# Optimization experiments

Hardware: AMD Instinct MI355X
Metric: run time of the kernel (lower is better)

Reference implementation:

```python
import jax, jax.numpy as jnp
import numpy as np

EPS = 1e-8
NUM_HEADS = 8


def setup_inputs() -> dict:
    key = jax.random.key(0)
    ks = jax.random.split(key, 12)
    B, T, F = 8, 512, 512
    H = NUM_HEADS
    dh = F // H
    maxlen = 2048
    s = 0.02  # weight init scale
    inp = {
        "x": jax.random.normal(ks[0], (B, T, F), jnp.float32),
        "Wq": jax.random.normal(ks[1], (F, F), jnp.float32) * s,
        "bq": jax.random.normal(ks[2], (F,), jnp.float32) * s,
        "Wk": jax.random.normal(ks[3], (F, F), jnp.float32) * s,
        "bk": jax.random.normal(ks[4], (F,), jnp.float32) * s,
        "Wv": jax.random.normal(ks[5], (F, F), jnp.float32) * s,
        "bv": jax.random.normal(ks[6], (F,), jnp.float32) * s,
        "Wo": jax.random.normal(ks[7], (F, F), jnp.float32) * s,
        "bo": jax.random.normal(ks[8], (F,), jnp.float32) * s,
        "delta": jnp.ones((1,), jnp.float32),
        "cache_k": jax.random.normal(ks[9], (B * H, maxlen, dh), jnp.float32) * 0.1,
        "cache_v": jax.random.normal(ks[10], (B * H, maxlen, dh), jnp.float32) * 0.1,
    }
    return inp


def _split_heads(t, H):
    # torch.cat(torch.split(t, dh, dim=-1), dim=0): head index outermost on dim 0
    B, T, F = t.shape
    dh = F // H
    return t.reshape(B, T, H, dh).transpose(2, 0, 1, 3).reshape(H * B, T, dh)


def _merge_heads(t, H):
    HB, T, dh = t.shape
    B = HB // H
    return t.reshape(H, B, T, dh).transpose(1, 2, 0, 3).reshape(B, T, H * dh)


def reference(x, Wq, bq, Wk, bk, Wv, bv, Wo, bo, delta, cache_k, cache_v):
    B, T, F = x.shape
    H = NUM_HEADS
    maxlen = cache_k.shape[1]
    d = jnp.sqrt(jnp.asarray(F, jnp.float32))

    q = _split_heads(x @ Wq.T + bq, H)  # [H*B, T, dh]
    k = _split_heads(x @ Wk.T + bk, H)
    v = _split_heads(x @ Wv.T + bv, H)

    # rolling KV cache: drop oldest T, append new T -> length maxlen
    k_full = jnp.concatenate([cache_k[:, T:], k], axis=1)  # [H*B, maxlen, dh]
    v_full = jnp.concatenate([cache_v[:, T:], v], axis=1)

    # Gaussian positional bias G = exp(-(i-j)^2 / (delta^2 + EPS)), last T rows
    i = jnp.arange(maxlen, dtype=jnp.float32)
    ind = -(i[:, None] - i[None, :]) ** 2  # [maxlen, maxlen]
    G = jnp.exp(ind[-T:] / (delta[0] ** 2 + EPS))  # [T, maxlen]

    scores = jnp.abs(jnp.einsum('btd,bsd->bts', q, k_full) * G / d)
    attn = jax.nn.softmax(scores, axis=-1)  # [H*B, T, maxlen]
    o = jnp.einsum('bts,bsd->btd', attn, v_full)  # [H*B, T, dh]

    out = _merge_heads(o, H) @ Wo.T + bo  # [B, T, F]
    return out
```

## Files before the change

kernel.cpp:

```cpp
#include <hip/hip_runtime.h>
#include <cstdint>
#include <cstddef>


typedef _Float16 f16x8 __attribute__((ext_vector_type(8)));
typedef _Float16 f16x4 __attribute__((ext_vector_type(4)));
typedef float f32x4 __attribute__((ext_vector_type(4)));

#define GLOBAL_AS __attribute__((address_space(1)))
#define LDS_AS __attribute__((address_space(3)))

__global__ void convert_f32_f16(const float* __restrict__ x,
                                const float* __restrict__ w0,
                                const float* __restrict__ w1,
                                const float* __restrict__ w2,
                                const float* __restrict__ w3,
                                _Float16* __restrict__ dst) {
  long e = ((long)blockIdx.x * 256 + threadIdx.x) * 4;
  const float* src;
  long off;
  if (e < 2097152) { src = x; off = 0; }
  else {
    int seg = (int)((e - 2097152) >> 18);
    src = seg == 0 ? w0 : seg == 1 ? w1 : seg == 2 ? w2 : w3;
    off = 2097152 + ((long)seg << 18);
  }
  float4 v = *(const float4*)(src + (e - off));
  f16x4 h;
  h[0] = (_Float16)v.x; h[1] = (_Float16)v.y;
  h[2] = (_Float16)v.z; h[3] = (_Float16)v.w;
  *(f16x4*)(dst + e) = h;
}

template <int MODE>
__launch_bounds__(256)
__global__ void gemm_nt(const _Float16* __restrict__ A,
                        const _Float16* __restrict__ B0,
                        const _Float16* __restrict__ B1,
                        const _Float16* __restrict__ B2,
                        const float* __restrict__ bias0,
                        const float* __restrict__ bias1,
                        const float* __restrict__ bias2,
                        void* out0v, void* out1v, void* out2v,
                        int K) {
  __shared__ __align__(16) _Float16 As[128 * 32];
  __shared__ __align__(16) _Float16 Bs[128 * 32];
  const int tid = threadIdx.x;
  const int m0 = blockIdx.x * 128;
  const int n0g = blockIdx.y * 128;

  const _Float16* Bsel;
  const float* bsel;
  void* oselv;
  int nloc0;
  if (MODE == 0) {
    int which = n0g >> 9;
    Bsel = which == 0 ? B0 : which == 1 ? B1 : B2;
    bsel = which == 0 ? bias0 : which == 1 ? bias1 : bias2;
    oselv = which == 0 ? out0v : which == 1 ? out1v : out2v;
    nloc0 = n0g & 511;
  } else {
    Bsel = B0; bsel = bias0; oselv = out0v; nloc0 = n0g;
  }

  const int w = tid >> 6, lane = tid & 63;
  const int wm = (w & 1) * 64, wn = (w >> 1) * 64;

  f32x4 acc[4][4];
#pragma unroll
  for (int i = 0; i < 4; i++)
#pragma unroll
    for (int j = 0; j < 4; j++) acc[i][j] = (f32x4){0.f, 0.f, 0.f, 0.f};

  for (int k0 = 0; k0 < K; k0 += 32) {
    __syncthreads();
#pragma unroll
    for (int r = 0; r < 2; r++) {
      int chunk = r * 256 + tid;
      int row = chunk >> 2;
      int c = (chunk & 3) * 8;
      const _Float16* ga = A + (size_t)(m0 + row) * K + k0 + c;
      const _Float16* gb = Bsel + (size_t)(nloc0 + row) * K + k0 + c;
      __builtin_amdgcn_global_load_lds((const GLOBAL_AS void*)ga,
                                       (LDS_AS void*)(As + chunk * 8), 16, 0, 0);
      __builtin_amdgcn_global_load_lds((const GLOBAL_AS void*)gb,
                                       (LDS_AS void*)(Bs + chunk * 8), 16, 0, 0);
    }
    __syncthreads();

    f16x8 af[4], bf[4];
#pragma unroll
    for (int i = 0; i < 4; i++) {
      af[i] = *(const f16x8*)(As + (wm + i * 16 + (lane & 15)) * 32 + (lane >> 4) * 8);
      bf[i] = *(const f16x8*)(Bs + (wn + i * 16 + (lane & 15)) * 32 + (lane >> 4) * 8);
    }
#pragma unroll
    for (int i = 0; i < 4; i++)
#pragma unroll
      for (int j = 0; j < 4; j++)
        acc[i][j] = __builtin_amdgcn_mfma_f32_16x16x32_f16(af[i], bf[j], acc[i][j], 0, 0, 0);
  }

  const int mbase = m0 + wm + ((lane >> 4) << 2);
  const int nbase = nloc0 + wn + (lane & 15);
#pragma unroll
  for (int i = 0; i < 4; i++) {
#pragma unroll
    for (int j = 0; j < 4; j++) {
      int fg = nbase + j * 16;
      float bv = bsel[fg];
#pragma unroll
      for (int r = 0; r < 4; r++) {
        int m = mbase + i * 16 + r;
        float val = acc[i][j][r] + bv;
        if (MODE == 0) {
          int h = fg >> 6, dd = fg & 63, b = m >> 9, t = m & 511;
          ((_Float16*)oselv)[(((size_t)((h << 3) + b) * 512 + t) << 6) + dd] =
              (_Float16)val;
        } else {
          ((float*)oselv)[(size_t)m * 512 + fg] = val;
        }
      }
    }
  }
}

__global__ void sum_v_partial(const float* __restrict__ cache_v,
                              const _Float16* __restrict__ v_new,
                              float* __restrict__ S_v) {
  const int hb = blockIdx.x;
  const int r0 = blockIdx.y * 128;
  const int d = threadIdx.x & 63, p = threadIdx.x >> 6;
  float s = 0.f;
#pragma unroll 8
  for (int r = r0 + p; r < r0 + 128; r += 4) {
    if (r < 1536)
      s += cache_v[((size_t)hb * 2048 + r + 512) * 64 + d];
    else
      s += (float)v_new[((size_t)hb * 512 + (r - 1536)) * 64 + d];
  }
  __shared__ float red[256];
  red[threadIdx.x] = s;
  __syncthreads();
  if (p == 0)
    atomicAdd(&S_v[hb * 64 + d], red[d] + red[64 + d] + red[128 + d] + red[192 + d]);
}

__launch_bounds__(256)
__global__ void attn_mfma(const _Float16* __restrict__ q,
                          const _Float16* __restrict__ k_new,
                          const _Float16* __restrict__ v_new,
                          const float* __restrict__ cache_k,
                          const float* __restrict__ cache_v,
                          const float* __restrict__ S_v,
                          const float* __restrict__ delta,
                          _Float16* __restrict__ o_merged) {
  const int hb = blockIdx.y;
  const int t0 = blockIdx.x * 64;
  const int jlo_t = 1520 + t0;

  __shared__ __align__(16) _Float16 Q_sh[64 * 72];
  __shared__ __align__(16) _Float16 K_sh[96 * 72];
  __shared__ __align__(16) _Float16 VT_sh[64 * 104];
  __shared__ __align__(16) _Float16 P_sh[64 * 104];
  __shared__ float S_sh[64 * 101];
  __shared__ float G_sh[40];
  __shared__ float pm_sh[256], ps_sh[256], em_sh[64], id_sh[64];

  const int tid = threadIdx.x;
  const int w = tid >> 6, lane = tid & 63;
  const float dscale = 0.044194173824159216f;

  if (tid < 36) {
    int di = tid - 16;
    float inv_g = 1.0f / (delta[0] * delta[0] + 1e-8f);
    G_sh[tid] = (tid <= 32) ? expf(-(float)(di * di) * inv_g) : 0.f;
  }
#pragma unroll
  for (int it = 0; it < 2; it++) {
    int idx = it * 256 + tid;
    int r = idx >> 3, c8 = (idx & 7) * 8;
    *(f16x8*)(Q_sh + r * 72 + c8) =
        *(const f16x8*)(q + ((size_t)hb * 512 + t0 + r) * 64 + c8);
  }
#pragma unroll
  for (int it = 0; it < 3; it++) {
    int idx = it * 256 + tid;
    int r = idx >> 3, c8 = (idx & 7) * 8;
    int j = jlo_t + r;
    f16x8 kh, vh;
    if (j < 1536) {
      const float* kp = cache_k + ((size_t)hb * 2048 + j + 512) * 64 + c8;
      const float* vp = cache_v + ((size_t)hb * 2048 + j + 512) * 64 + c8;
#pragma unroll
      for (int e = 0; e < 8; e++) {
        kh[e] = (_Float16)kp[e];
        vh[e] = (_Float16)vp[e];
      }
    } else if (j < 2048) {
      kh = *(const f16x8*)(k_new + ((size_t)hb * 512 + (j - 1536)) * 64 + c8);
      vh = *(const f16x8*)(v_new + ((size_t)hb * 512 + (j - 1536)) * 64 + c8);
    } else {
#pragma unroll
      for (int e = 0; e < 8; e++) { kh[e] = (_Float16)0.f; vh[e] = (_Float16)0.f; }
    }
    *(f16x8*)(K_sh + r * 72 + c8) = kh;
#pragma unroll
    for (int e = 0; e < 8; e++) VT_sh[(c8 + e) * 104 + r] = vh[e];
  }
  for (int idx = tid; idx < 832; idx += 256) {
    int r = idx / 13, c = (idx % 13) * 8;
    *(f16x8*)(P_sh + r * 104 + c) = (f16x8){0, 0, 0, 0, 0, 0, 0, 0};
  }
  __syncthreads();

  {
    const int mrow = w * 16 + (lane & 15);
    const int koff = (lane >> 4) * 8;
    f16x8 aq0 = *(const f16x8*)(Q_sh + mrow * 72 + koff);
    f16x8 aq1 = *(const f16x8*)(Q_sh + mrow * 72 + 32 + koff);
    f32x4 accS[6];
#pragma unroll
    for (int n = 0; n < 6; n++) accS[n] = (f32x4){0.f, 0.f, 0.f, 0.f};
#pragma unroll
    for (int n = 0; n < 6; n++) {
      f16x8 b0 = *(const f16x8*)(K_sh + (n * 16 + (lane & 15)) * 72 + koff);
      f16x8 b1 = *(const f16x8*)(K_sh + (n * 16 + (lane & 15)) * 72 + 32 + koff);
      accS[n] = __builtin_amdgcn_mfma_f32_16x16x32_f16(aq0, b0, accS[n], 0, 0, 0);
      accS[n] = __builtin_amdgcn_mfma_f32_16x16x32_f16(aq1, b1, accS[n], 0, 0, 0);
    }
#pragma unroll
    for (int n = 0; n < 6; n++)
#pragma unroll
      for (int r = 0; r < 4; r++) {
        int tl = w * 16 + ((lane >> 4) << 2) + r;
        int jb = n * 16 + (lane & 15);
        S_sh[tl * 101 + jb] = fabsf(accS[n][r]) * dscale;
      }
  }
  __syncthreads();

  {
    const int tl = lane;
    const int jmax = 2047 - (jlo_t + tl);
    float s[9];
    float pm = 0.f;
#pragma unroll
    for (int jj = 0; jj < 9; jj++) {
      int off = w * 9 + jj;
      bool valid = (off <= 32) && (off <= jmax);
      s[jj] = valid ? S_sh[tl * 101 + tl + off] * G_sh[off] : 0.f;
      pm = fmaxf(pm, s[jj]);
    }
    pm_sh[w * 64 + tl] = pm;
    __syncthreads();
    float m = fmaxf(fmaxf(pm_sh[tl], pm_sh[64 + tl]),
                    fmaxf(pm_sh[128 + tl], pm_sh[192 + tl]));
    float em = expf(-m);
    float ps = 0.f;
#pragma unroll
    for (int jj = 0; jj < 9; jj++) {
      int off = w * 9 + jj;
      bool valid = (off <= 32) && (off <= jmax);
      float wgt = valid ? (expf(s[jj] - m) - em) : 0.f;
      ps += wgt;
      if (valid) P_sh[tl * 104 + tl + off] = (_Float16)wgt;
    }
    ps_sh[w * 64 + tl] = ps;
    __syncthreads();
    if (w == 0) {
      float sw = ps_sh[tl] + ps_sh[64 + tl] + ps_sh[128 + tl] + ps_sh[192 + tl];
      em_sh[tl] = em;
      id_sh[tl] = 1.0f / (sw + 2048.f * em);
    }
  }

  f32x4 accO[4];
#pragma unroll
  for (int mi = 0; mi < 4; mi++) accO[mi] = (f32x4){0.f, 0.f, 0.f, 0.f};
  {
    const int koff = (lane >> 4) * 8;
    const int nrow = w * 16 + (lane & 15);
#pragma unroll
    for (int k = 0; k < 3; k++) {
      f16x8 bv = *(const f16x8*)(VT_sh + nrow * 104 + k * 32 + koff);
#pragma unroll
      for (int mi = 0; mi < 4; mi++) {
        f16x8 ap = *(const f16x8*)(P_sh + (mi * 16 + (lane & 15)) * 104 + k * 32 + koff);
        accO[mi] = __builtin_amdgcn_mfma_f32_16x16x32_f16(ap, bv, accO[mi], 0, 0, 0);
      }
    }
  }
  __syncthreads();

  const int h = hb >> 3, b = hb & 7;
  const int d = w * 16 + (lane & 15);
  const float svd = S_v[hb * 64 + d];
#pragma unroll
  for (int mi = 0; mi < 4; mi++)
#pragma unroll
    for (int r = 0; r < 4; r++) {
      int trow = mi * 16 + ((lane >> 4) << 2) + r;
      float val = (accO[mi][r] + em_sh[trow] * svd) * id_sh[trow];
      o_merged[((size_t)(b * 512 + t0 + trow)) * 512 + h * 64 + d] = (_Float16)val;
    }
}

extern "C" void kernel_launch(void* const* d_in, const int* in_sizes, int n_in,
                              void* d_out, int out_size, void* d_ws, size_t ws_size,
                              hipStream_t stream) {
  const float* x = (const float*)d_in[0];
  const float* Wq = (const float*)d_in[1];
  const float* bq = (const float*)d_in[2];
  const float* Wk = (const float*)d_in[3];
  const float* bk = (const float*)d_in[4];
  const float* Wv = (const float*)d_in[5];
  const float* bv = (const float*)d_in[6];
  const float* Wo = (const float*)d_in[7];
  const float* bo = (const float*)d_in[8];
  const float* delta = (const float*)d_in[9];
  const float* cache_k = (const float*)d_in[10];
  const float* cache_v = (const float*)d_in[11];
  float* out = (float*)d_out;

  _Float16* xh = (_Float16*)d_ws;
  _Float16* Wqh = xh + 2097152;
  _Float16* Wkh = Wqh + 262144;
  _Float16* Wvh = Wkh + 262144;
  _Float16* Woh = Wvh + 262144;
  _Float16* qf = Woh + 262144;
  _Float16* kf = qf + 2097152;
  _Float16* vf = kf + 2097152;
  float* sv = (float*)(vf + 2097152);
  _Float16* oh = (_Float16*)(sv + 4096);

  convert_f32_f16<<<3072, 256, 0, stream>>>(x, Wq, Wk, Wv, Wo, xh);

  dim3 g1(32, 12);
  gemm_nt<0><<<g1, 256, 0, stream>>>(xh, Wqh, Wkh, Wvh, bq, bk, bv,
                                     (void*)qf, (void*)kf, (void*)vf, 512);

  hipMemsetAsync(sv, 0, 64 * 64 * sizeof(float), stream);
  dim3 gs(64, 16);
  sum_v_partial<<<gs, 256, 0, stream>>>(cache_v, vf, sv);

  dim3 g2(8, 64);
  attn_mfma<<<g2, 256, 0, stream>>>(qf, kf, vf, cache_k, cache_v, sv, delta, oh);

  dim3 g3(32, 4);
  gemm_nt<1><<<g3, 256, 0, stream>>>(oh, Woh, nullptr, nullptr, bo, nullptr, nullptr,
                                     (void*)out, nullptr, nullptr, 512);
}
```

Before: 170.0 us.

## Fuse cache_v sum into prep kernel, shrink GEMM tiles, drop atomics and memset

The conversion kernel now also computes partial sums of the cached V rows, written to per-chunk slots rather than accumulated with atomics. This removes the memset, and a small kernel sums the new V rows after the QKV GEMM. The attention kernel reduces the 20 partials itself and loads the K/V tail with float4 reads. Both GEMMs use smaller N tiles (and a 64x64 tile for the output projection), giving more blocks to fill the GPU. The risk is lower per-block data reuse in the GEMMs and extra partial-reduction work in every attention block.

```diff
diff --git a/kernel.cpp b/kernel.cpp
--- a/kernel.cpp
+++ b/kernel.cpp
@@ -10,140 +10,141 @@
 #define GLOBAL_AS __attribute__((address_space(1)))
 #define LDS_AS __attribute__((address_space(3)))
 
-__global__ void convert_f32_f16(const float* __restrict__ x,
-                                const float* __restrict__ w0,
-                                const float* __restrict__ w1,
-                                const float* __restrict__ w2,
-                                const float* __restrict__ w3,
-                                _Float16* __restrict__ dst) {
-  long e = ((long)blockIdx.x * 256 + threadIdx.x) * 4;
-  const float* src;
-  long off;
-  if (e < 2097152) { src = x; off = 0; }
-  else {
-    int seg = (int)((e - 2097152) >> 18);
-    src = seg == 0 ? w0 : seg == 1 ? w1 : seg == 2 ? w2 : w3;
-    off = 2097152 + ((long)seg << 18);
-  }
-  float4 v = *(const float4*)(src + (e - off));
-  f16x4 h;
-  h[0] = (_Float16)v.x; h[1] = (_Float16)v.y;
-  h[2] = (_Float16)v.z; h[3] = (_Float16)v.w;
-  *(f16x4*)(dst + e) = h;
-}
-
-template <int MODE>
 __launch_bounds__(256)
-__global__ void gemm_nt(const _Float16* __restrict__ A,
-                        const _Float16* __restrict__ B0,
-                        const _Float16* __restrict__ B1,
-                        const _Float16* __restrict__ B2,
-                        const float* __restrict__ bias0,
-                        const float* __restrict__ bias1,
-                        const float* __restrict__ bias2,
-                        void* out0v, void* out1v, void* out2v,
-                        int K) {
-  __shared__ __align__(16) _Float16 As[128 * 32];
-  __shared__ __align__(16) _Float16 Bs[128 * 32];
+__global__ void prep(const float* __restrict__ x,
+                     const float* __restrict__ Wq, const float* __restrict__ Wk,
+                     const float* __restrict__ Wv, const float* __restrict__ Wo,
+                     const float* __restrict__ cache_v,
+                     _Float16* __restrict__ xh, _Float16* __restrict__ wh,
+                     float* __restrict__ part) {
+  const int bid = blockIdx.x;
   const int tid = threadIdx.x;
-  const int m0 = blockIdx.x * 128;
-  const int n0g = blockIdx.y * 128;
-
-  const _Float16* Bsel;
-  const float* bsel;
-  void* oselv;
-  int nloc0;
-  if (MODE == 0) {
-    int which = n0g >> 9;
-    Bsel = which == 0 ? B0 : which == 1 ? B1 : B2;
-    bsel = which == 0 ? bias0 : which == 1 ? bias1 : bias2;
-    oselv = which == 0 ? out0v : which == 1 ? out1v : out2v;
-    nloc0 = n0g & 511;
+  if (bid < 2048) {
+    long e = ((long)bid * 256 + tid) * 4;
+    float4 v = *(const float4*)(x + e);
+    f16x4 h;
+    h[0] = (_Float16)v.x; h[1] = (_Float16)v.y;
+    h[2] = (_Float16)v.z; h[3] = (_Float16)v.w;
+    *(f16x4*)(xh + e) = h;
+  } else if (bid < 3072) {
+    long e = ((long)(bid - 2048) * 256 + tid) * 4;
+    int seg = (int)(e >> 18);
+    const float* w = seg == 0 ? Wq : seg == 1 ? Wk : seg == 2 ? Wv : Wo;
+    float4 v = *(const float4*)(w + (e & 262143));
+    f16x4 h;
+    h[0] = (_Float16)v.x; h[1] = (_Float16)v.y;
+    h[2] = (_Float16)v.z; h[3] = (_Float16)v.w;
+    *(f16x4*)(wh + e) = h;
   } else {
-    Bsel = B0; bsel = bias0; oselv = out0v; nloc0 = n0g;
-  }
-
-  const int w = tid >> 6, lane = tid & 63;
-  const int wm = (w & 1) * 64, wn = (w >> 1) * 64;
-
-  f32x4 acc[4][4];
-#pragma unroll
-  for (int i = 0; i < 4; i++)
-#pragma unroll
-    for (int j = 0; j < 4; j++) acc[i][j] = (f32x4){0.f, 0.f, 0.f, 0.f};
-
-  for (int k0 = 0; k0 < K; k0 += 32) {
-    __syncthreads();
-#pragma unroll
-    for (int r = 0; r < 2; r++) {
-      int chunk = r * 256 + tid;
-      int row = chunk >> 2;
-      int c = (chunk & 3) * 8;
-      const _Float16* ga = A + (size_t)(m0 + row) * K + k0 + c;
-      const _Float16* gb = Bsel + (size_t)(nloc0 + row) * K + k0 + c;
-      __builtin_amdgcn_global_load_lds((const GLOBAL_AS void*)ga,
-                                       (LDS_AS void*)(As + chunk * 8), 16, 0, 0);
-      __builtin_amdgcn_global_load_lds((const GLOBAL_AS void*)gb,
-                                       (LDS_AS void*)(Bs + chunk * 8), 16, 0, 0);
-    }
-    __syncthreads();
-
-    f16x8 af[4], bf[4];
-#pragma unroll
-    for (int i = 0; i < 4; i++) {
-      af[i] = *(const f16x8*)(As + (wm + i * 16 + (lane & 15)) * 32 + (lane >> 4) * 8);
-      bf[i] = *(const f16x8*)(Bs + (wn + i * 16 + (lane & 15)) * 32 + (lane >> 4) * 8);
-    }
-#pragma unroll
-    for (int i = 0; i < 4; i++)
-#pragma unroll
-      for (int j = 0; j < 4; j++)
-        acc[i][j] = __builtin_amdgcn_mfma_f32_16x16x32_f16(af[i], bf[j], acc[i][j], 0, 0, 0);
-  }
-
-  const int mbase = m0 + wm + ((lane >> 4) << 2);
-  const int nbase = nloc0 + wn + (lane & 15);
-#pragma unroll
-  for (int i = 0; i < 4; i++) {
-#pragma unroll
-    for (int j = 0; j < 4; j++) {
-      int fg = nbase + j * 16;
-      float bv = bsel[fg];
-#pragma unroll
-      for (int r = 0; r < 4; r++) {
-        int m = mbase + i * 16 + r;
-        float val = acc[i][j][r] + bv;
-        if (MODE == 0) {
-          int h = fg >> 6, dd = fg & 63, b = m >> 9, t = m & 511;
-          ((_Float16*)oselv)[(((size_t)((h << 3) + b) * 512 + t) << 6) + dd] =
-              (_Float16)val;
-        } else {
-          ((float*)oselv)[(size_t)m * 512 + fg] = val;
-        }
-      }
-    }
-  }
-}
-
-__global__ void sum_v_partial(const float* __restrict__ cache_v,
-                              const _Float16* __restrict__ v_new,
-                              float* __restrict__ S_v) {
-  const int hb = blockIdx.x;
-  const int r0 = blockIdx.y * 128;
-  const int d = threadIdx.x & 63, p = threadIdx.x >> 6;
+    int pb = bid - 3072;
+    int hb = pb >> 4, chunk = pb & 15;
+    int d = tid & 63, p = tid >> 6;
+    int r0 = 512 + chunk * 96;
+    float s = 0.f;
+    for (int r = r0 + p; r < r0 + 96; r += 4)
+      s += cache_v[((size_t)hb * 2048 + r) * 64 + d];
+    __shared__ float red[256];
+    red[tid] = s;
+    __syncthreads();
+    if (p == 0)
+      part[(hb * 20 + chunk) * 64 + d] =
+          red[d] + red[64 + d] + red[128 + d] + red[192 + d];
+  }
+}
+
+__launch_bounds__(256)
+__global__ void sumv_new(const _Float16* __restrict__ v_new,
+                         float* __restrict__ part) {
+  int hb = blockIdx.x >> 2, chunk = blockIdx.x & 3;
+  int d = threadIdx.x & 63, p = threadIdx.x >> 6;
+  int r0 = chunk * 128;
   float s = 0.f;
-#pragma unroll 8
-  for (int r = r0 + p; r < r0 + 128; r += 4) {
-    if (r < 1536)
-      s += cache_v[((size_t)hb * 2048 + r + 512) * 64 + d];
-    else
-      s += (float)v_new[((size_t)hb * 512 + (r - 1536)) * 64 + d];
-  }
+  for (int r = r0 + p; r < r0 + 128; r += 4)
+    s += (float)v_new[((size_t)hb * 512 + r) * 64 + d];
   __shared__ float red[256];
   red[threadIdx.x] = s;
   __syncthreads();
   if (p == 0)
-    atomicAdd(&S_v[hb * 64 + d], red[d] + red[64 + d] + red[128 + d] + red[192 + d]);
+    part[(hb * 20 + 16 + chunk) * 64 + d] =
+        red[d] + red[64 + d] + red[128 + d] + red[192 + d];
+}
+
+__launch_bounds__(256)
+__global__ void gemm_qkv(const _Float16* __restrict__ xh,
+                         const _Float16* __restrict__ wh,
+                         const float* __restrict__ bq,
+                         const float* __restrict__ bk,
+                         const float* __restrict__ bv,
+                         _Float16* __restrict__ q, _Float16* __restrict__ k,
+                         _Float16* __restrict__ v) {
+  __shared__ __align__(16) _Float16 As[128 * 32];
+  __shared__ __align__(16) _Float16 Bs[64 * 32];
+  const int tid = threadIdx.x;
+  const int m0 = blockIdx.x * 128;
+  const int n0g = blockIdx.y * 64;
+  const int which = n0g >> 9;
+  const int nloc0 = n0g & 511;
+  const _Float16* Bsel = wh + (size_t)which * 262144;
+  const float* bsel = which == 0 ? bq : which == 1 ? bk : bv;
+  _Float16* osel = which == 0 ? q : which == 1 ? k : v;
+  const int w = tid >> 6, lane = tid & 63;
+  const int wm = (w & 1) * 64, wn = (w >> 1) * 32;
+
+  f32x4 acc[4][2];
+#pragma unroll
+  for (int i = 0; i < 4; i++)
+#pragma unroll
+    for (int j = 0; j < 2; j++) acc[i][j] = (f32x4){0.f, 0.f, 0.f, 0.f};
+
+  for (int k0 = 0; k0 < 512; k0 += 32) {
+    __syncthreads();
+#pragma unroll
+    for (int r = 0; r < 2; r++) {
+      int c = r * 256 + tid;
+      int row = c >> 2, c8 = (c & 3) * 8;
+      __builtin_amdgcn_global_load_lds(
+          (const GLOBAL_AS void*)(xh + (size_t)(m0 + row) * 512 + k0 + c8),
+          (LDS_AS void*)(As + c * 8), 16, 0, 0);
+    }
+    {
+      int row = tid >> 2, c8 = (tid & 3) * 8;
+      __builtin_amdgcn_global_load_lds(
+          (const GLOBAL_AS void*)(Bsel + (size_t)(nloc0 + row) * 512 + k0 + c8),
+          (LDS_AS void*)(Bs + tid * 8), 16, 0, 0);
+    }
+    __syncthreads();
+
+    f16x8 af[4], bf[2];
+#pragma unroll
+    for (int i = 0; i < 4; i++)
+      af[i] = *(const f16x8*)(As + (wm + i * 16 + (lane & 15)) * 32 + (lane >> 4) * 8);
+#pragma unroll
+    for (int j = 0; j < 2; j++)
+      bf[j] = *(const f16x8*)(Bs + (wn + j * 16 + (lane & 15)) * 32 + (lane >> 4) * 8);
+#pragma unroll
+    for (int i = 0; i < 4; i++)
+#pragma unroll
+      for (int j = 0; j < 2; j++)
+        acc[i][j] = __builtin_amdgcn_mfma_f32_16x16x32_f16(af[i], bf[j], acc[i][j], 0, 0, 0);
+  }
+
+  const int mbase = m0 + wm + ((lane >> 4) << 2);
+  const int nbase = nloc0 + wn + (lane & 15);
+#pragma unroll
+  for (int i = 0; i < 4; i++)
+#pragma unroll
+    for (int j = 0; j < 2; j++) {
+      int fg = nbase + j * 16;
+      float bv2 = bsel[fg];
+      int h = fg >> 6, dd = fg & 63;
+#pragma unroll
+      for (int r = 0; r < 4; r++) {
+        int m = mbase + i * 16 + r;
+        int b = m >> 9, t = m & 511;
+        osel[(((size_t)((h << 3) + b) * 512 + t) << 6) + dd] =
+            (_Float16)(acc[i][j][r] + bv2);
+      }
+    }
 }
 
 __launch_bounds__(256)
@@ -152,7 +153,7 @@
                           const _Float16* __restrict__ v_new,
                           const float* __restrict__ cache_k,
                           const float* __restrict__ cache_v,
-                          const float* __restrict__ S_v,
+                          const float* __restrict__ part,
                           const float* __restrict__ delta,
                           _Float16* __restrict__ o_merged) {
   const int hb = blockIdx.y;
@@ -165,7 +166,7 @@
   __shared__ __align__(16) _Float16 P_sh[64 * 104];
   __shared__ float S_sh[64 * 101];
   __shared__ float G_sh[40];
-  __shared__ float pm_sh[256], ps_sh[256], em_sh[64], id_sh[64];
+  __shared__ float pm_sh[256], ps_sh[256], em_sh[64], id_sh[64], sv_sh[64];
 
   const int tid = threadIdx.x;
   const int w = tid >> 6, lane = tid & 63;
@@ -175,6 +176,13 @@
     int di = tid - 16;
     float inv_g = 1.0f / (delta[0] * delta[0] + 1e-8f);
     G_sh[tid] = (tid <= 32) ? expf(-(float)(di * di) * inv_g) : 0.f;
+  }
+  if (tid >= 64 && tid < 128) {
+    int d = tid - 64;
+    float s = 0.f;
+#pragma unroll
+    for (int c = 0; c < 20; c++) s += part[(hb * 20 + c) * 64 + d];
+    sv_sh[d] = s;
   }
 #pragma unroll
   for (int it = 0; it < 2; it++) {
@@ -184,29 +192,28 @@
         *(const f16x8*)(q + ((size_t)hb * 512 + t0 + r) * 64 + c8);
   }
 #pragma unroll
-  for (int it = 0; it < 3; it++) {
+  for (int it = 0; it < 6; it++) {
     int idx = it * 256 + tid;
-    int r = idx >> 3, c8 = (idx & 7) * 8;
+    int r = idx >> 4, c4 = idx & 15;
     int j = jlo_t + r;
-    f16x8 kh, vh;
+    f16x4 kh, vh;
     if (j < 1536) {
-      const float* kp = cache_k + ((size_t)hb * 2048 + j + 512) * 64 + c8;
-      const float* vp = cache_v + ((size_t)hb * 2048 + j + 512) * 64 + c8;
-#pragma unroll
-      for (int e = 0; e < 8; e++) {
-        kh[e] = (_Float16)kp[e];
-        vh[e] = (_Float16)vp[e];
-      }
+      float4 k4 = *(const float4*)(cache_k + ((size_t)hb * 2048 + j + 512) * 64 + c4 * 4);
+      float4 v4 = *(const float4*)(cache_v + ((size_t)hb * 2048 + j + 512) * 64 + c4 * 4);
+      kh[0] = (_Float16)k4.x; kh[1] = (_Float16)k4.y;
+      kh[2] = (_Float16)k4.z; kh[3] = (_Float16)k4.w;
+      vh[0] = (_Float16)v4.x; vh[1] = (_Float16)v4.y;
+      vh[2] = (_Float16)v4.z; vh[3] = (_Float16)v4.w;
     } else if (j < 2048) {
-      kh = *(const f16x8*)(k_new + ((size_t)hb * 512 + (j - 1536)) * 64 + c8);
-      vh = *(const f16x8*)(v_new + ((size_t)hb * 512 + (j - 1536)) * 64 + c8);
+      kh = *(const f16x4*)(k_new + ((size_t)hb * 512 + (j - 1536)) * 64 + c4 * 4);
+      vh = *(const f16x4*)(v_new + ((size_t)hb * 512 + (j - 1536)) * 64 + c4 * 4);
     } else {
 #pragma unroll
-      for (int e = 0; e < 8; e++) { kh[e] = (_Float16)0.f; vh[e] = (_Float16)0.f; }
-    }
-    *(f16x8*)(K_sh + r * 72 + c8) = kh;
-#pragma unroll
-    for (int e = 0; e < 8; e++) VT_sh[(c8 + e) * 104 + r] = vh[e];
+      for (int e = 0; e < 4; e++) { kh[e] = (_Float16)0.f; vh[e] = (_Float16)0.f; }
+    }
+    *(f16x4*)(K_sh + r * 72 + c4 * 4) = kh;
+#pragma unroll
+    for (int e = 0; e < 4; e++) VT_sh[(c4 * 4 + e) * 104 + r] = vh[e];
   }
   for (int idx = tid; idx < 832; idx += 256) {
     int r = idx / 13, c = (idx % 13) * 8;
@@ -295,7 +302,7 @@
 
   const int h = hb >> 3, b = hb & 7;
   const int d = w * 16 + (lane & 15);
-  const float svd = S_v[hb * 64 + d];
+  const float svd = sv_sh[d];
 #pragma unroll
   for (int mi = 0; mi < 4; mi++)
 #pragma unroll
@@ -303,6 +310,68 @@
       int trow = mi * 16 + ((lane >> 4) << 2) + r;
       float val = (accO[mi][r] + em_sh[trow] * svd) * id_sh[trow];
       o_merged[((size_t)(b * 512 + t0 + trow)) * 512 + h * 64 + d] = (_Float16)val;
+    }
+}
+
+__launch_bounds__(256)
+__global__ void gemm_out(const _Float16* __restrict__ A,
+                         const _Float16* __restrict__ Bw,
+                         const float* __restrict__ bias,
+                         float* __restrict__ out) {
+  __shared__ __align__(16) _Float16 As[64 * 32];
+  __shared__ __align__(16) _Float16 Bs[64 * 32];
+  const int tid = threadIdx.x;
+  const int m0 = blockIdx.x * 64;
+  const int n0 = blockIdx.y * 64;
+  const int w = tid >> 6, lane = tid & 63;
+  const int wm = (w & 1) * 32, wn = (w >> 1) * 32;
+
+  f32x4 acc[2][2];
+#pragma unroll
+  for (int i = 0; i < 2; i++)
+#pragma unroll
+    for (int j = 0; j < 2; j++) acc[i][j] = (f32x4){0.f, 0.f, 0.f, 0.f};
+
+  for (int k0 = 0; k0 < 512; k0 += 32) {
+    __syncthreads();
+    {
+      int row = tid >> 2, c8 = (tid & 3) * 8;
+      __builtin_amdgcn_global_load_lds(
+          (const GLOBAL_AS void*)(A + (size_t)(m0 + row) * 512 + k0 + c8),
+          (LDS_AS void*)(As + tid * 8), 16, 0, 0);
+      __builtin_amdgcn_global_load_lds(
+          (const GLOBAL_AS void*)(Bw + (size_t)(n0 + row) * 512 + k0 + c8),
+          (LDS_AS void*)(Bs + tid * 8), 16, 0, 0);
+    }
+    __syncthreads();
+
+    f16x8 af[2], bf[2];
+#pragma unroll
+    for (int i = 0; i < 2; i++)
+      af[i] = *(const f16x8*)(As + (wm + i * 16 + (lane & 15)) * 32 + (lane >> 4) * 8);
+#pragma unroll
+    for (int j = 0; j < 2; j++)
+      bf[j] = *(const f16x8*)(Bs + (wn + j * 16 + (lane & 15)) * 32 + (lane >> 4) * 8);
+#pragma unroll
+    for (int i = 0; i < 2; i++)
+#pragma unroll
+      for (int j = 0; j < 2; j++)
+        acc[i][j] = __builtin_amdgcn_mfma_f32_16x16x32_f16(af[i], bf[j], acc[i][j], 0, 0, 0);
+  }
+
+  const int mbase = m0 + wm + ((lane >> 4) << 2);
+  const int nbase = n0 + wn + (lane & 15);
+#pragma unroll
+  for (int i = 0; i < 2; i++)
+#pragma unroll
+    for (int j = 0; j < 2; j++) {
+      int fg = nbase + j * 16;
+      float bv = bias[fg];
+#pragma unroll
+      for (int r = 0; r < 4; r++) {
+        int m = mbase + i * 16 + r;
+        out[(size_t)m * 512 + fg] = acc[i][j][r] + bv;
+      }
     }
 }
 
@@ -324,30 +393,23 @@
   float* out = (float*)d_out;
 
   _Float16* xh = (_Float16*)d_ws;
-  _Float16* Wqh = xh + 2097152;
-  _Float16* Wkh = Wqh + 262144;
-  _Float16* Wvh = Wkh + 262144;
-  _Float16* Woh = Wvh + 262144;
-  _Float16* qf = Woh + 262144;
+  _Float16* wh = xh + 2097152;
+  _Float16* qf = wh + 1048576;
   _Float16* kf = qf + 2097152;
   _Float16* vf = kf + 2097152;
-  float* sv = (float*)(vf + 2097152);
-  _Float16* oh = (_Float16*)(sv + 4096);
-
-  convert_f32_f16<<<3072, 256, 0, stream>>>(x, Wq, Wk, Wv, Wo, xh);
-
-  dim3 g1(32, 12);
-  gemm_nt<0><<<g1, 256, 0, stream>>>(xh, Wqh, Wkh, Wvh, bq, bk, bv,
-                                     (void*)qf, (void*)kf, (void*)vf, 512);
-
-  hipMemsetAsync(sv, 0, 64 * 64 * sizeof(float), stream);
-  dim3 gs(64, 16);
-  sum_v_partial<<<gs, 256, 0, stream>>>(cache_v, vf, sv);
+  float* part = (float*)(vf + 2097152);
+  _Float16* oh = (_Float16*)(part + 81920);
+
+  prep<<<4096, 256, 0, stream>>>(x, Wq, Wk, Wv, Wo, cache_v, xh, wh, part);
+
+  dim3 g1(32, 24);
+  gemm_qkv<<<g1, 256, 0, stream>>>(xh, wh, bq, bk, bv, qf, kf, vf);
+
+  sumv_new<<<256, 256, 0, stream>>>(vf, part);
 
   dim3 g2(8, 64);
-  attn_mfma<<<g2, 256, 0, stream>>>(qf, kf, vf, cache_k, cache_v, sv, delta, oh);
-
-  dim3 g3(32, 4);
-  gemm_nt<1><<<g3, 256, 0, stream>>>(oh, Woh, nullptr, nullptr, bo, nullptr, nullptr,
-                                     (void*)out, nullptr, nullptr, 512);
-}
+  attn_mfma<<<g2, 256, 0, stream>>>(qf, kf, vf, cache_k, cache_v, part, delta, oh);
+
+  dim3 g3(64, 8);
+  gemm_out<<<g3, 256, 0, stream>>>(oh, wh + 3 * 262144, bo, out);
+}
```

Measured after the change: 163.9 us. 1.04x faster.
